# Optimization experiments

Hardware: AMD Instinct MI355X
Metric: run time of the kernel (lower is better)

## Reference

```python
import jax, jax.numpy as jnp
import numpy as np

MAX_LEVEL = 3
FULL_LEN = 2 ** MAX_LEVEL  # wavelet_full_len for db1, mode='zero'


def _make_patterns():
    # Per-feature input to the DWT is [v, 0, ..., 0] (scalar zero-padded to 2**j).
    # Haar/db1 'zero' DWT of that signal is v times a fixed sparse pattern:
    # cA (len 1) = v*2^(-j/2); cD_k first element = v*2^(-k/2), rest zeros.
    pats = []
    for j in range(1, MAX_LEVEL + 1):
        vec = [2.0 ** (-j / 2.0)]                      # cA, length 1
        for k in range(1, j + 1):                      # cD_1 .. cD_j
            seg = np.zeros(2 ** (j - k))
            seg[0] = 2.0 ** (-k / 2.0)
            vec.extend(seg.tolist())
        full = np.zeros(FULL_LEN, dtype=np.float32)
        arr = np.asarray(vec, dtype=np.float32)
        full[: arr.shape[0]] = arr                     # F.pad to wavelet_full_len
        pats.append(full)
    return jnp.asarray(np.stack(pats))                 # (MAX_LEVEL, FULL_LEN)

_P = _make_patterns()


def _gumbel_hard(logits, gumb):
    # F.gumbel_softmax(logits, tau=1.0, hard=True), one sample per feature row.
    y = jax.nn.softmax(logits[None, :] + gumb, axis=-1)          # (feat, L)
    hard = jax.nn.one_hot(jnp.argmax(y, axis=-1), y.shape[-1], dtype=y.dtype)
    return jax.lax.stop_gradient(hard - y) + y                   # straight-through


def _wavelet_layer(x, logits, gumb, Wnl, bnl, Wwo, bwo):
    # Collapses the per-feature/per-level torch double loop:
    # xi_wave(level j) = v * (Wnl[f] . P[j]) + bnl[f]
    a = Wnl @ _P.T                       # (feat, levels)
    w = _gumbel_hard(logits, gumb)       # (feat, levels), one-hot rows
    coeff = jnp.sum(w * a, axis=-1)      # (feat,)
    agg = x * coeff + bnl                # (B, N, feat)
    return agg @ Wwo + bwo               # linear_out


def _mix(h, res_proj):
    diff = jnp.mean((h - res_proj) ** 2)
    th = jax.nn.sigmoid(diff)
    return th * h + (1.0 - th) * res_proj


def reference(x, adj, Wres, bres,
              Wg0, bg0, Wrg0, brg0, logits0, gumb0, Wnl0, bnl0, Wwo0, bwo0, Wrw0, brw0,
              Wg1, bg1, Wrg1, brg1, logits1, gumb1, Wnl1, bnl1, Wwo1, bwo1, Wrw1, brw1):
    res = x @ Wres + bres                                        # (B,N,Dout)
    # ---- layer 0 ----
    xg = jnp.einsum('ij,bjf->bif', adj, x) @ Wg0 + bg0           # 64->256: no residual add
    xg = _mix(xg, res @ Wrg0 + brg0)
    xw = _wavelet_layer(xg, logits0, gumb0, Wnl0, bnl0, Wwo0, bwo0) + xg  # 256==256: add
    xw = _mix(xw, res @ Wrw0 + brw0)
    # ---- layer 1 ----
    xg1 = jnp.einsum('ij,bjf->bif', adj, xw) @ Wg1 + bg1 + xw    # 256==256: add
    xg1 = _mix(xg1, res @ Wrg1 + brg1)
    xw1 = _wavelet_layer(xg1, logits1, gumb1, Wnl1, bnl1, Wwo1, bwo1)     # 256->64: no add
    xw1 = _mix(xw1, res @ Wrw1 + brw1)
    return xw1


def setup_inputs() -> dict:
    key = jax.random.key(0)
    ks = jax.random.split(key, 32)
    B, N, D_in, H, D_out = 128, 512, 64, 256, 64
    s = 0.05
    inp = {
        'x': jax.random.normal(ks[0], (B, N, D_in), jnp.float32),
        'adj': jax.random.uniform(ks[1], (N, N), jnp.float32) / N,
        'Wres': jax.random.normal(ks[2], (D_in, D_out), jnp.float32) * s,
        'bres': jax.random.normal(ks[3], (D_out,), jnp.float32) * s,
        'Wg0': jax.random.normal(ks[4], (D_in, H), jnp.float32) * s,
        'bg0': jax.random.normal(ks[5], (H,), jnp.float32) * s,
        'Wrg0': jax.random.normal(ks[6], (D_out, H), jnp.float32) * s,
        'brg0': jax.random.normal(ks[7], (H,), jnp.float32) * s,
        'logits0': jax.random.normal(ks[8], (3,), jnp.float32),
        'gumb0': jax.random.gumbel(ks[9], (H, 3), jnp.float32),
        'Wnl0': jax.random.normal(ks[10], (H, FULL_LEN), jnp.float32) * s,
        'bnl0': jax.random.normal(ks[11], (H,), jnp.float32) * s,
        'Wwo0': jax.random.normal(ks[12], (H, H), jnp.float32) * s,
        'bwo0': jax.random.normal(ks[13], (H,), jnp.float32) * s,
        'Wrw0': jax.random.normal(ks[14], (D_out, H), jnp.float32) * s,
        'brw0': jax.random.normal(ks[15], (H,), jnp.float32) * s,
        'Wg1': jax.random.normal(ks[16], (H, H), jnp.float32) * s,
        'bg1': jax.random.normal(ks[17], (H,), jnp.float32) * s,
        'Wrg1': jax.random.normal(ks[18], (D_out, H), jnp.float32) * s,
        'brg1': jax.random.normal(ks[19], (H,), jnp.float32) * s,
        'logits1': jax.random.normal(ks[20], (3,), jnp.float32),
        'gumb1': jax.random.gumbel(ks[21], (H, 3), jnp.float32),
        'Wnl1': jax.random.normal(ks[22], (H, FULL_LEN), jnp.float32) * s,
        'bnl1': jax.random.normal(ks[23], (H,), jnp.float32) * s,
        'Wwo1': jax.random.normal(ks[24], (H, D_out), jnp.float32) * s,
        'bwo1': jax.random.normal(ks[25], (D_out,), jnp.float32) * s,
        'Wrw1': jax.random.normal(ks[26], (D_out, D_out), jnp.float32) * s,
        'brw1': jax.random.normal(ks[27], (D_out,), jnp.float32) * s,
    }
    return inp
```

## Files before the change

### kernel.cpp

```cpp
#include <hip/hip_runtime.h>
#include <hip/hip_bf16.h>
#include <math.h>

#define BB   128
#define NN   512
#define DIN  64
#define HH   256
#define DOUT 64
#define BNR  (BB * NN)

typedef float  f32x4  __attribute__((ext_vector_type(4)));
typedef __bf16 bf16x8 __attribute__((ext_vector_type(8)));

#define GLP(p)  ((const __attribute__((address_space(1))) void*)(p))
#define LDSP(p) ((__attribute__((address_space(3))) void*)(p))

__constant__ float PAT[3][8] = {
    {0.70710678f, 0.70710678f, 0.f, 0.f, 0.f, 0.f, 0.f, 0.f},
    {0.5f,        0.70710678f, 0.f, 0.5f, 0.f, 0.f, 0.f, 0.f},
    {0.35355339f, 0.70710678f, 0.f, 0.f, 0.f, 0.5f, 0.f, 0.35355339f}
};

__device__ __forceinline__ unsigned short f2bfu(float x) {
    __hip_bfloat16 b = __float2bfloat16(x);
    unsigned short u;
    __builtin_memcpy(&u, &b, 2);
    return u;
}
__device__ __forceinline__ float bf2f(unsigned short u) {
    unsigned int v = ((unsigned int)u) << 16;
    float f;
    __builtin_memcpy(&f, &v, 4);
    return f;
}

__device__ __forceinline__ float block_th(const float* __restrict__ partial, int np,
                                          float inv_n, float* red, int tid)
{
    float s = 0.f;
    for (int i = tid; i < np; i += 256) s += partial[i];
    red[tid] = s;
    __syncthreads();
    for (int o = 128; o > 0; o >>= 1) {
        if (tid < o) red[tid] += red[tid + o];
        __syncthreads();
    }
    float th = 1.f / (1.f + expf(-red[0] * inv_n));
    __syncthreads();
    return th;
}

template<int BM, int BN, int FM, int FN>
__device__ __forceinline__ void write_tile(char* lds, f32x4 (&a)[FM][FN],
                                           __hip_bfloat16* __restrict__ C,
                                           long base, int N, int tid)
{
    const int wave = tid >> 6;
    const int lane = tid & 63;
    const int wm = wave >> 1, wn = wave & 1;
    const int lc = lane & 15;
    const int lr4 = (lane >> 4) << 2;
    __syncthreads();
    #pragma unroll
    for (int j = 0; j < FN; ++j) {
        int colb = (wn * (FN * 16) + j * 16 + lc) * 2;
        #pragma unroll
        for (int i = 0; i < FM; ++i) {
            int row0 = wm * (FM * 16) + i * 16 + lr4;
            #pragma unroll
            for (int r = 0; r < 4; ++r) {
                int row = row0 + r;
                *reinterpret_cast<unsigned short*>(
                    lds + row * (BN * 2) + (colb ^ (((row >> 2) & 3) << 5))) =
                    f2bfu(a[i][j][r]);
            }
        }
    }
    __syncthreads();
    const int TPR = BN / 8;
    const int RPP = 256 / TPR;
    #pragma unroll
    for (int p = 0; p < BM / RPP; ++p) {
        int row = p * RPP + tid / TPR;
        int cb = (tid % TPR) * 16;
        int pb = cb ^ (((row >> 2) & 3) << 5);
        uint4 v = *reinterpret_cast<const uint4*>(lds + row * (BN * 2) + pb);
        *reinterpret_cast<uint4*>(reinterpret_cast<char*>(C + base + (long)row * N) + cb) = v;
    }
}

template<int BM, int BN, int FM, int FN>
__device__ __forceinline__ void write_tileT(char* lds, f32x4 (&a)[FM][FN],
                                            __hip_bfloat16* __restrict__ CT,
                                            long baseT, int ldT, int tid)
{
    const int wave = tid >> 6;
    const int lane = tid & 63;
    const int wm = wave >> 1, wn = wave & 1;
    const int lc = lane & 15;
    const int lr4 = (lane >> 4) << 2;
    __syncthreads();
    #pragma unroll
    for (int j = 0; j < FN; ++j) {
        int c = wn * (FN * 16) + j * 16 + lc;
        int cbase = c * (BM * 2);
        int swz = ((c >> 2) & 3) << 5;
        #pragma unroll
        for (int i = 0; i < FM; ++i) {
            int m0 = wm * (FM * 16) + i * 16 + lr4;
            #pragma unroll
            for (int r = 0; r < 4; ++r) {
                int m = m0 + r;
                *reinterpret_cast<unsigned short*>(lds + cbase + ((m * 2) ^ swz)) =
                    f2bfu(a[i][j][r]);
            }
        }
    }
    __syncthreads();
    const int TPR = BM / 8;
    const int RPP = 256 / TPR;
    #pragma unroll
    for (int p = 0; p < BN / RPP; ++p) {
        int c = p * RPP + tid / TPR;
        int tb = (tid % TPR) * 16;
        int pb = tb ^ (((c >> 2) & 3) << 5);
        uint4 v = *reinterpret_cast<const uint4*>(lds + c * (BM * 2) + pb);
        *reinterpret_cast<uint4*>(reinterpret_cast<char*>(CT + baseT + (long)c * ldT) + tb) = v;
    }
}

template<int BM, int BN>
__device__ __forceinline__ void stage_tiles(const __hip_bfloat16* __restrict__ Ab,
                                            const __hip_bfloat16* __restrict__ Bb,
                                            char* AsB, char* BsB,
                                            int m0, int n0, int k0, int KA, int KB,
                                            int wave, int lane)
{
    const int NCH = (BM + BN) / 32;
    const int lr = lane >> 3;
    const int ls = lane & 7;
    #pragma unroll
    for (int cc = 0; cc < NCH; ++cc) {
        int c = wave * NCH + cc;
        const __hip_bfloat16* src;
        char* ldsb;
        if (c < BM / 8) {
            int r = c * 8 + lr;
            ldsb = AsB + c * 1024;
            src = Ab + ((long)(m0 + r) * KA + k0 + ((ls ^ (r & 7)) << 3));
        } else {
            int c2 = c - BM / 8;
            int r = c2 * 8 + lr;
            ldsb = BsB + c2 * 1024;
            src = Bb + ((long)(n0 + r) * KB + k0 + ((ls ^ (r & 7)) << 3));
        }
        __builtin_amdgcn_global_load_lds(GLP(src), LDSP(ldsb), 16, 0, 0);
    }
}

template<int BM, int BN, int FM, int FN>
__device__ __forceinline__ void mfma_tiles(char* AsB, char* BsB,
                                           f32x4 (&acc)[FM][FN], int wave, int lane)
{
    const int wm = wave >> 1, wn = wave & 1;
    #pragma unroll
    for (int ksl = 0; ksl < 2; ++ksl) {
        bf16x8 af[FM], bfr[FN];
        #pragma unroll
        for (int i = 0; i < FM; ++i) {
            int row = wm * (FM * 16) + i * 16 + (lane & 15);
            int off = (ksl * 64 + ((lane >> 4) << 4)) ^ ((row & 7) << 4);
            af[i] = *reinterpret_cast<const bf16x8*>(AsB + row * 128 + off);
        }
        #pragma unroll
        for (int j = 0; j < FN; ++j) {
            int row = wn * (FN * 16) + j * 16 + (lane & 15);
            int off = (ksl * 64 + ((lane >> 4) << 4)) ^ ((row & 7) << 4);
            bfr[j] = *reinterpret_cast<const bf16x8*>(BsB + row * 128 + off);
        }
        #pragma unroll
        for (int i = 0; i < FM; ++i)
            #pragma unroll
            for (int j = 0; j < FN; ++j)
                acc[i][j] = __builtin_amdgcn_mfma_f32_16x16x32_bf16(
                    af[i], bfr[j], acc[i][j], 0, 0, 0);
    }
}

__global__ __launch_bounds__(256) void cvta_k(const float* __restrict__ adj,
                                              unsigned int* __restrict__ adjb,
                                              float* __restrict__ ars)
{
    int n = blockIdx.x;
    int t = threadIdx.x;
    float2 v = reinterpret_cast<const float2*>(adj)[n * 256 + t];
    adjb[n * 256 + t] = (unsigned int)f2bfu(v.x) | ((unsigned int)f2bfu(v.y) << 16);
    __shared__ float sm[256];
    sm[t] = v.x + v.y;
    __syncthreads();
    for (int o = 128; o > 0; o >>= 1) {
        if (t < o) sm[t] += sm[t + o];
        __syncthreads();
    }
    if (t == 0) ars[n] = sm[0];
}

__global__ __launch_bounds__(256) void cvtx_k(const float* __restrict__ in,
                                              unsigned short* __restrict__ rm,
                                              unsigned short* __restrict__ tr)
{
    __shared__ float t[64][65];
    const long base = (long)blockIdx.z * NN * DIN;
    const int r0 = blockIdx.y * 64;
    const int tr4 = threadIdx.x >> 6;
    const int tc  = threadIdx.x & 63;
    #pragma unroll
    for (int i = 0; i < 16; ++i) {
        int r = i * 4 + tr4;
        float v = in[base + (long)(r0 + r) * DIN + tc];
        t[r][tc] = v;
        rm[base + (long)(r0 + r) * DIN + tc] = f2bfu(v);
    }
    __syncthreads();
    #pragma unroll
    for (int i = 0; i < 16; ++i) {
        int d = i * 4 + tr4;
        tr[base + (long)d * NN + r0 + tc] = f2bfu(t[tc][d]);
    }
}

__device__ __forceinline__ void tcvt_body(const float* __restrict__ in,
                                          unsigned short* __restrict__ out,
                                          const float* __restrict__ cs, float us,
                                          int R, int C, int r0, int c0)
{
    __shared__ float t[64][65];
    int tr = threadIdx.x >> 6;
    int tc = threadIdx.x & 63;
    #pragma unroll
    for (int i = 0; i < 16; ++i) {
        int r = i * 4 + tr;
        t[r][tc] = in[(long)(r0 + r) * C + c0 + tc];
    }
    __syncthreads();
    float sc = (cs ? cs[r0 + tc] : 1.0f) * us;
    #pragma unroll
    for (int i = 0; i < 16; ++i) {
        int r = i * 4 + tr;
        out[(long)(c0 + r) * R + r0 + tc] = f2bfu(t[tc][r] * sc);
    }
}

struct WTArgs {
    const float* src[8];
    unsigned short* dst[8];
    const float* cs[8];
    float sgn[8];
    int R[8], C[8];
};
__global__ __launch_bounds__(256) void tcvt_w_k(WTArgs a)
{
    int wgt = blockIdx.y;
    int R = a.R[wgt], C = a.C[wgt];
    int tilesX = C >> 6;
    int tiles = (R >> 6) * tilesX;
    int t = blockIdx.x;
    if (t >= tiles) return;
    tcvt_body(a.src[wgt], a.dst[wgt], a.cs[wgt], a.sgn[wgt], R, C,
              (t / tilesX) * 64, (t % tilesX) * 64);
}

__global__ void coeff2_k(const float* __restrict__ logits0, const float* __restrict__ gumb0,
                         const float* __restrict__ Wnl0, float* __restrict__ c0,
                         const float* __restrict__ logits1, const float* __restrict__ gumb1,
                         const float* __restrict__ Wnl1, float* __restrict__ c1)
{
    const float* lg = blockIdx.x ? logits1 : logits0;
    const float* gb = blockIdx.x ? gumb1 : gumb0;
    const float* Wn = blockIdx.x ? Wnl1 : Wnl0;
    float* cc = blockIdx.x ? c1 : c0;
    int f = threadIdx.x;
    float l0 = lg[0] + gb[f * 3 + 0];
    float l1 = lg[1] + gb[f * 3 + 1];
    float l2 = lg[2] + gb[f * 3 + 2];
    int bl = 0;
    float bv = l0;
    if (l1 > bv) { bv = l1; bl = 1; }
    if (l2 > bv) { bv = l2; bl = 2; }
    float s = 0.f;
    #pragma unroll
    for (int t = 0; t < 8; ++t) s += Wn[f * 8 + t] * PAT[bl][t];
    cc[f] = s;
}

struct FVArgs {
    const float* W[6];
    const float* c[6];
    const float* v[6];
    const float* base[6];
    float* out[6];
    int K[6], N[6];
};
__global__ __launch_bounds__(256) void foldvec_k(FVArgs a)
{
    int cs = blockIdx.y;
    int n = blockIdx.x;
    if (n >= a.N[cs]) return;
    int k = threadIdx.x;
    float s = 0.f;
    if (k < a.K[cs]) {
        float cc = a.c[cs] ? a.c[cs][k] : 1.0f;
        s = a.v[cs][k] * cc * a.W[cs][(long)k * a.N[cs] + n];
    }
    __shared__ float sm[256];
    sm[threadIdx.x] = s;
    __syncthreads();
    for (int o = 128; o > 0; o >>= 1) {
        if (threadIdx.x < o) sm[threadIdx.x] += sm[threadIdx.x + o];
        __syncthreads();
    }
    if (threadIdx.x == 0)
        a.out[cs][n] = (a.base[cs] ? a.base[cs][n] : 0.f) + sm[0];
}

struct WFArgs {
    const float* Wsrc[4];
    const float* Wbig[4];
    const float* c[4];
    int incl[4], N[4];
    unsigned short* dst[4];
};
__global__ __launch_bounds__(256) void wfold_k(WFArgs a)
{
    int cs = blockIdx.y;
    int m = blockIdx.x;
    __shared__ float ws[256];
    const float* c = a.c[cs];
    ws[threadIdx.x] = a.Wsrc[cs][m * 256 + threadIdx.x] * (c ? c[threadIdx.x] : 1.0f);
    __syncthreads();
    int n = threadIdx.x;
    int N = a.N[cs];
    if (n >= N) return;
    float s = a.incl[cs] ? a.Wsrc[cs][m * 256 + n] : 0.f;
    const float* Wb = a.Wbig[cs];
    #pragma unroll 8
    for (int k = 0; k < 256; ++k)
        s += ws[k] * Wb[(long)k * N + n];
    a.dst[cs][n * 64 + m] = f2bfu(s);
}

__global__ __launch_bounds__(256) void sc0_k(
    const float* __restrict__ partial, int np, float inv_n,
    unsigned short* __restrict__ Wa,
    unsigned short* __restrict__ Wb,
    const float* __restrict__ bg0p, const float* __restrict__ brg0p,
    const float* __restrict__ crow0, float* __restrict__ cv0)
{
    __shared__ float red[256];
    float th = block_th(partial, np, inv_n, red, threadIdx.x);
    float om = 1.f - th;
    int g = blockIdx.x * 256 + threadIdx.x;
    Wa[g] = f2bfu(th * bf2f(Wa[g]));
    Wb[g] = f2bfu(om * bf2f(Wb[g]));
    if (g < 256) cv0[g] = th * bg0p[g] + om * brg0p[g] + crow0[g];
}

__global__ __launch_bounds__(256) void sc1_k(
    const float* __restrict__ partial, int np, float inv_n,
    unsigned short* __restrict__ Wg1T,
    const unsigned short* __restrict__ Wrw0T, unsigned short* __restrict__ Wrw0sT,
    unsigned short* __restrict__ Wg0pT, unsigned short* __restrict__ Wrg0pT,
    unsigned short* __restrict__ WrwWg1T,
    const float* __restrict__ bg1, const float* __restrict__ brw0,
    const float* __restrict__ cv0, const float* __restrict__ bw1v,
    float* __restrict__ bv1g, float* __restrict__ bw1s)
{
    __shared__ float red[256];
    float th = block_th(partial, np, inv_n, red, threadIdx.x);
    float om = 1.f - th;
    int g = blockIdx.x * 256 + threadIdx.x;
    Wg1T[g] = f2bfu(th * bf2f(Wg1T[g]));
    if (g < 16384) {
        Wrw0sT[g]  = f2bfu(om * bf2f(Wrw0T[g]));
        Wg0pT[g]   = f2bfu(th * bf2f(Wg0pT[g]));
        Wrg0pT[g]  = f2bfu(th * bf2f(Wrg0pT[g]));
        WrwWg1T[g] = f2bfu(om * bf2f(WrwWg1T[g]));
    }
    if (g < 256) {
        bv1g[g] = bg1[g] + om * brw0[g] + th * cv0[g];
        bw1s[g] = om * bw1v[g];
    }
}

__global__ __launch_bounds__(256) void sc2_k(
    const float* __restrict__ partial, int np, float inv_n,
    unsigned short* __restrict__ Wc1T,
    unsigned short* __restrict__ Wrgc1T,
    const float* __restrict__ brgc1, const float* __restrict__ crow1,
    float* __restrict__ cv2)
{
    __shared__ float red[256];
    float th = block_th(partial, np, inv_n, red, threadIdx.x);
    float om = 1.f - th;
    int g = blockIdx.x * 256 + threadIdx.x;
    Wc1T[g] = f2bfu(th * bf2f(Wc1T[g]));
    if (g < 4096) Wrgc1T[g] = f2bfu(om * bf2f(Wrgc1T[g]));
    if (g < 64) cv2[g] = om * brgc1[g] + crow1[g];
}

template<int BM, int BN, int FM, int FN>
__global__ __launch_bounds__(256) void gemm_res_k(
    const __hip_bfloat16* __restrict__ A, const __hip_bfloat16* __restrict__ Bt,
    const float* __restrict__ bias,
    __hip_bfloat16* __restrict__ Cb, __hip_bfloat16* __restrict__ CbT,
    int M, int N, int K)
{
    __shared__ __attribute__((aligned(128))) char lds[(BM + BN) * 128];
    char* AsB = lds;
    char* BsB = lds + BM * 128;

    const int m0 = blockIdx.y * BM;
    const int n0 = 0;
    const int tid  = threadIdx.x;
    const int wave = tid >> 6;
    const int lane = tid & 63;
    const int wn = wave & 1;

    f32x4 acc[FM][FN];
    #pragma unroll
    for (int i = 0; i < FM; ++i)
        #pragma unroll
        for (int j = 0; j < FN; ++j)
            acc[i][j] = (f32x4){0.f, 0.f, 0.f, 0.f};

    for (int k0 = 0; k0 < K; k0 += 64) {
        stage_tiles<BM, BN>(A, Bt, AsB, BsB, m0, n0, k0, K, K, wave, lane);
        __syncthreads();
        mfma_tiles<BM, BN, FM, FN>(AsB, BsB, acc, wave, lane);
        __syncthreads();
    }

    const int lc = lane & 15;
    #pragma unroll
    for (int j = 0; j < FN; ++j) {
        float bv = bias[n0 + wn * (FN * 16) + j * 16 + lc];
        #pragma unroll
        for (int i = 0; i < FM; ++i)
            #pragma unroll
            for (int r = 0; r < 4; ++r)
                acc[i][j][r] += bv;
    }
    write_tile<BM, BN, FM, FN>(lds, acc, Cb, (long)m0 * N + n0, N, tid);
    long baseT = (long)(m0 / NN) * ((long)N * NN) + (m0 % NN);
    write_tileT<BM, BN, FM, FN>(lds, acc, CbT, baseT, NN, tid);
}

template<int BM, int BN, int FM, int FN, int GX, int NB>
__global__ __launch_bounds__(256) void gemm_bt_swz_k(
    const __hip_bfloat16* __restrict__ A, const __hip_bfloat16* __restrict__ Bt,
    __hip_bfloat16* __restrict__ Cb,
    int M, int N, int K, long sA, long sB, long sC)
{
    __shared__ __attribute__((aligned(128))) char lds[(BM + BN) * 128];
    char* AsB = lds;
    char* BsB = lds + BM * 128;

    const int d   = blockIdx.x;
    const int xcd = d & 7;
    const int q   = d >> 3;
    const int t   = q % NB;
    const int bz  = xcd + ((q / NB) << 3);
    const int n0  = (t % GX) * BN;
    const int m0  = (t / GX) * BM;

    const __hip_bfloat16* Ab = A + (long)bz * sA;
    const __hip_bfloat16* Bb = Bt + (long)bz * sB;

    const int tid  = threadIdx.x;
    const int wave = tid >> 6;
    const int lane = tid & 63;

    f32x4 acc[FM][FN];
    #pragma unroll
    for (int i = 0; i < FM; ++i)
        #pragma unroll
        for (int j = 0; j < FN; ++j)
            acc[i][j] = (f32x4){0.f, 0.f, 0.f, 0.f};

    for (int k0 = 0; k0 < K; k0 += 64) {
        stage_tiles<BM, BN>(Ab, Bb, AsB, BsB, m0, n0, k0, K, K, wave, lane);
        __syncthreads();
        mfma_tiles<BM, BN, FM, FN>(AsB, BsB, acc, wave, lane);
        __syncthreads();
    }

    write_tile<BM, BN, FM, FN>(lds, acc, Cb, (long)bz * sC + (long)m0 * N + n0, N, tid);
}

template<int BM, int BN, int FM, int FN>
__global__ __launch_bounds__(256) void dual1_k(
    const __hip_bfloat16* __restrict__ A0, const __hip_bfloat16* __restrict__ B0, int K0,
    const __hip_bfloat16* __restrict__ A1, const __hip_bfloat16* __restrict__ B1, int K1,
    const float* __restrict__ b1, const float* __restrict__ b2,
    float* __restrict__ partial, int M, int N)
{
    __shared__ __attribute__((aligned(128))) char lds[(BM + BN) * 128];
    char* AsB = lds;
    char* BsB = lds + BM * 128;

    const int d   = blockIdx.x;
    const int q   = d >> 3;
    const int nx  = q & 1;
    const int my  = (d & 7) + ((q >> 1) << 3);
    const int m0  = my * BM;
    const int n0  = nx * BN;

    const int tid  = threadIdx.x;
    const int wave = tid >> 6;
    const int lane = tid & 63;
    const int wn = wave & 1;

    f32x4 acc[FM][FN];
    #pragma unroll
    for (int i = 0; i < FM; ++i)
        #pragma unroll
        for (int j = 0; j < FN; ++j)
            acc[i][j] = (f32x4){0.f, 0.f, 0.f, 0.f};

    #pragma unroll
    for (int ph = 0; ph < 2; ++ph) {
        const __hip_bfloat16* Ab = ph ? A1 : A0;
        const __hip_bfloat16* Bb = ph ? B1 : B0;
        const int K = ph ? K1 : K0;
        for (int k0 = 0; k0 < K; k0 += 64) {
            stage_tiles<BM, BN>(Ab, Bb, AsB, BsB, m0, n0, k0, K, K, wave, lane);
            __syncthreads();
            mfma_tiles<BM, BN, FM, FN>(AsB, BsB, acc, wave, lane);
            __syncthreads();
        }
    }

    const int lc = lane & 15;
    float dsum = 0.f;
    #pragma unroll
    for (int j = 0; j < FN; ++j) {
        int col = n0 + wn * (FN * 16) + j * 16 + lc;
        float bd = b1[col] - b2[col];
        #pragma unroll
        for (int i = 0; i < FM; ++i)
            #pragma unroll
            for (int r = 0; r < 4; ++r) {
                float dd = acc[i][j][r] + bd;
                dsum += dd * dd;
            }
    }

    float* red = (float*)lds;
    red[tid] = dsum;
    __syncthreads();
    for (int o = 128; o > 0; o >>= 1) {
        if (tid < o) red[tid] += red[tid + o];
        __syncthreads();
    }
    if (tid == 0) partial[my * 2 + nx] = red[0];
}

template<int BM, int BN, int FM, int FN>
__global__ __launch_bounds__(256) void wave2T_k(
    const __hip_bfloat16* __restrict__ A0, const __hip_bfloat16* __restrict__ B0, int K0,
    const __hip_bfloat16* __restrict__ A1, const __hip_bfloat16* __restrict__ B1, int K1,
    const __hip_bfloat16* __restrict__ A2, const __hip_bfloat16* __restrict__ B2, int K2,
    const float* __restrict__ cv, const float* __restrict__ b2v,
    __hip_bfloat16* __restrict__ C1T, float* __restrict__ partial_out, int M, int N)
{
    __shared__ __attribute__((aligned(128))) char lds[(BM + BN) * 128];
    char* AsB = lds;
    char* BsB = lds + BM * 128;

    const int d   = blockIdx.x;
    const int q   = d >> 3;
    const int nx  = q & 1;
    const int my  = (d & 7) + ((q >> 1) << 3);
    const int m0  = my * BM;
    const int n0  = nx * BN;

    const int tid  = threadIdx.x;
    const int wave = tid >> 6;
    const int lane = tid & 63;
    const int wn = wave & 1;

    f32x4 acc0[FM][FN], acc1[FM][FN];
    #pragma unroll
    for (int i = 0; i < FM; ++i)
        #pragma unroll
        for (int j = 0; j < FN; ++j) {
            acc0[i][j] = (f32x4){0.f, 0.f, 0.f, 0.f};
            acc1[i][j] = (f32x4){0.f, 0.f, 0.f, 0.f};
        }

    #pragma unroll
    for (int ph = 0; ph < 3; ++ph) {
        const __hip_bfloat16* Ab = (ph == 0) ? A0 : (ph == 1 ? A1 : A2);
        const __hip_bfloat16* Bb = (ph == 0) ? B0 : (ph == 1 ? B1 : B2);
        const int K = (ph == 0) ? K0 : (ph == 1 ? K1 : K2);
        for (int k0 = 0; k0 < K; k0 += 64) {
            stage_tiles<BM, BN>(Ab, Bb, AsB, BsB, m0, n0, k0, K, K, wave, lane);
            __syncthreads();
            if (ph < 2) mfma_tiles<BM, BN, FM, FN>(AsB, BsB, acc0, wave, lane);
            else        mfma_tiles<BM, BN, FM, FN>(AsB, BsB, acc1, wave, lane);
            __syncthreads();
        }
    }

    const int lc = lane & 15;
    float dsum = 0.f;
    #pragma unroll
    for (int j = 0; j < FN; ++j) {
        int col = n0 + wn * (FN * 16) + j * 16 + lc;
        float c1 = cv[col];
        float c2 = b2v[col];
        #pragma unroll
        for (int i = 0; i < FM; ++i)
            #pragma unroll
            for (int r = 0; r < 4; ++r) {
                float v1 = acc0[i][j][r] + c1;
                float v2 = acc1[i][j][r] + c2;
                acc0[i][j][r] = v1;
                float dd = v1 - v2;
                dsum += dd * dd;
            }
    }

    float* red = (float*)lds;
    red[tid] = dsum;
    __syncthreads();
    for (int o = 128; o > 0; o >>= 1) {
        if (tid < o) red[tid] += red[tid + o];
        __syncthreads();
    }
    if (tid == 0) partial_out[my * 2 + nx] = red[0];

    long baseT = (long)(m0 / NN) * ((long)N * NN) + (long)n0 * NN + (m0 % NN);
    write_tileT<BM, BN, FM, FN>(lds, acc0, C1T, baseT, NN, tid);
}

template<int BM, int BN, int FM, int FN>
__global__ __launch_bounds__(256) void gmix4_k(
    const __hip_bfloat16* __restrict__ A0, const __hip_bfloat16* __restrict__ B0, int K0,
    const __hip_bfloat16* __restrict__ A1, const __hip_bfloat16* __restrict__ B1, int K1,
    const __hip_bfloat16* __restrict__ A2, const __hip_bfloat16* __restrict__ B2, int K2,
    const __hip_bfloat16* __restrict__ A3, const __hip_bfloat16* __restrict__ B3, int K3,
    const __hip_bfloat16* __restrict__ A4, const __hip_bfloat16* __restrict__ B4, int K4,
    const __hip_bfloat16* __restrict__ A5, const __hip_bfloat16* __restrict__ B5, int K5,
    const float* __restrict__ bv1, const float* __restrict__ b2v,
    const float* __restrict__ ars, const float* __restrict__ bw1s,
    __hip_bfloat16* __restrict__ C1, float* __restrict__ partial_out, int M, int N)
{
    __shared__ __attribute__((aligned(128))) char lds[(BM + BN) * 128];
    char* AsB = lds;
    char* BsB = lds + BM * 128;

    const int d  = blockIdx.x;
    const int q  = d >> 3;
    const int nx = q & 1;
    const int my = (d & 7) + ((q >> 1) << 3);
    const int m0 = my * BM;
    const int n0 = nx * BN;

    const int tid  = threadIdx.x;
    const int wave = tid >> 6;
    const int lane = tid & 63;
    const int wm = wave >> 1, wn = wave & 1;

    f32x4 acc0[FM][FN], acc1[FM][FN];
    #pragma unroll
    for (int i = 0; i < FM; ++i)
        #pragma unroll
        for (int j = 0; j < FN; ++j) {
            acc0[i][j] = (f32x4){0.f, 0.f, 0.f, 0.f};
            acc1[i][j] = (f32x4){0.f, 0.f, 0.f, 0.f};
        }

    const __hip_bfloat16* As[6] = {A0, A1, A2, A3, A4, A5};
    const __hip_bfloat16* Bs[6] = {B0, B1, B2, B3, B4, B5};
    const int Ks[6] = {K0, K1, K2, K3, K4, K5};

    #pragma unroll
    for (int ph = 0; ph < 6; ++ph) {
        const __hip_bfloat16* Ab = As[ph];
        const __hip_bfloat16* Bb = Bs[ph];
        const int K = Ks[ph];
        for (int k0 = 0; k0 < K; k0 += 64) {
            stage_tiles<BM, BN>(Ab, Bb, AsB, BsB, m0, n0, k0, K, K, wave, lane);
            __syncthreads();
            if (ph < 5) mfma_tiles<BM, BN, FM, FN>(AsB, BsB, acc0, wave, lane);
            else        mfma_tiles<BM, BN, FM, FN>(AsB, BsB, acc1, wave, lane);
            __syncthreads();
        }
    }

    const int lc  = lane & 15;
    const int lr4 = (lane >> 4) << 2;
    const int node0 = m0 & (NN - 1);
    float dsum = 0.f;
    #pragma unroll
    for (int j = 0; j < FN; ++j) {
        int col = n0 + wn * (FN * 16) + j * 16 + lc;
        float c1 = bv1[col];
        float c2 = b2v[col];
        float bw = bw1s[col];
        #pragma unroll
        for (int i = 0; i < FM; ++i) {
            int rowl = wm * (FM * 16) + i * 16 + lr4;
            #pragma unroll
            for (int r = 0; r < 4; ++r) {
                float av = ars[node0 + rowl + r];
                float v1 = acc0[i][j][r] + c1 + av * bw;
                float v2 = acc1[i][j][r] + c2;
                acc0[i][j][r] = v1;
                float dd = v1 - v2;
                dsum += dd * dd;
            }
        }
    }

    float* red = (float*)lds;
    red[tid] = dsum;
    __syncthreads();
    for (int o = 128; o > 0; o >>= 1) {
        if (tid < o) red[tid] += red[tid + o];
        __syncthreads();
    }
    if (tid == 0) partial_out[my * 2 + nx] = red[0];

    write_tile<BM, BN, FM, FN>(lds, acc0, C1, (long)m0 * N + n0, N, tid);
}

template<int BM, int BN, int FM, int FN>
__global__ __launch_bounds__(256) void wave2_k(
    const __hip_bfloat16* __restrict__ A0, const __hip_bfloat16* __restrict__ B0, int K0,
    const __hip_bfloat16* __restrict__ A1, const __hip_bfloat16* __restrict__ B1, int K1,
    const __hip_bfloat16* __restrict__ A2, const __hip_bfloat16* __restrict__ B2, int K2,
    const float* __restrict__ cv, const float* __restrict__ b2v,
    __hip_bfloat16* __restrict__ C1, __hip_bfloat16* __restrict__ C2,
    float* __restrict__ partial_out, int M, int N)
{
    __shared__ __attribute__((aligned(128))) char lds[(BM + BN) * 128];
    char* AsB = lds;
    char* BsB = lds + BM * 128;

    const int m0 = blockIdx.y * BM;
    const int n0 = blockIdx.x * BN;
    const int pidx = blockIdx.y * gridDim.x + blockIdx.x;

    const int tid  = threadIdx.x;
    const int wave = tid >> 6;
    const int lane = tid & 63;
    const int wn = wave & 1;

    f32x4 acc0[FM][FN], acc1[FM][FN];
    #pragma unroll
    for (int i = 0; i < FM; ++i)
        #pragma unroll
        for (int j = 0; j < FN; ++j) {
            acc0[i][j] = (f32x4){0.f, 0.f, 0.f, 0.f};
            acc1[i][j] = (f32x4){0.f, 0.f, 0.f, 0.f};
        }

    #pragma unroll
    for (int ph = 0; ph < 3; ++ph) {
        const __hip_bfloat16* Ab = (ph == 0) ? A0 : (ph == 1 ? A1 : A2);
        const __hip_bfloat16* Bb = (ph == 0) ? B0 : (ph == 1 ? B1 : B2);
        const int K = (ph == 0) ? K0 : (ph == 1 ? K1 : K2);
        for (int k0 = 0; k0 < K; k0 += 64) {
            stage_tiles<BM, BN>(Ab, Bb, AsB, BsB, m0, n0, k0, K, K, wave, lane);
            __syncthreads();
            if (ph < 2) mfma_tiles<BM, BN, FM, FN>(AsB, BsB, acc0, wave, lane);
            else        mfma_tiles<BM, BN, FM, FN>(AsB, BsB, acc1, wave, lane);
            __syncthreads();
        }
    }

    const int lc = lane & 15;
    float dsum = 0.f;
    #pragma unroll
    for (int j = 0; j < FN; ++j) {
        int col = n0 + wn * (FN * 16) + j * 16 + lc;
        float c1 = cv[col];
        float c2 = b2v[col];
        #pragma unroll
        for (int i = 0; i < FM; ++i)
            #pragma unroll
            for (int r = 0; r < 4; ++r) {
                float v1 = acc0[i][j][r] + c1;
                float v2 = acc1[i][j][r] + c2;
                acc0[i][j][r] = v1;
                acc1[i][j][r] = v2;
                float dd = v1 - v2;
                dsum += dd * dd;
            }
    }

    float* red = (float*)lds;
    red[tid] = dsum;
    __syncthreads();
    for (int o = 128; o > 0; o >>= 1) {
        if (tid < o) red[tid] += red[tid + o];
        __syncthreads();
    }
    if (tid == 0) partial_out[pidx] = red[0];

    write_tile<BM, BN, FM, FN>(lds, acc0, C1, (long)m0 * N + n0, N, tid);
    write_tile<BM, BN, FM, FN>(lds, acc1, C2, (long)m0 * N + n0, N, tid);
}

__global__ __launch_bounds__(256) void mixfinal_k(
    const unsigned short* __restrict__ h, const unsigned short* __restrict__ r,
    const float* __restrict__ partial_in, int np_in, float inv_in,
    float* __restrict__ out, long n4)
{
    __shared__ float sm[256];
    const float th = block_th(partial_in, np_in, inv_in, sm, (int)threadIdx.x);
    const float om = 1.f - th;
    long gid = (long)blockIdx.x * 256 + threadIdx.x;
    long stride = (long)gridDim.x * 256;
    for (long i = gid; i < n4; i += stride) {
        ushort4 hv = reinterpret_cast<const ushort4*>(h)[i];
        ushort4 rv = reinterpret_cast<const ushort4*>(r)[i];
        float4 o;
        o.x = th * bf2f(hv.x) + om * bf2f(rv.x);
        o.y = th * bf2f(hv.y) + om * bf2f(rv.y);
        o.z = th * bf2f(hv.z) + om * bf2f(rv.z);
        o.w = th * bf2f(hv.w) + om * bf2f(rv.w);
        reinterpret_cast<float4*>(out)[i] = o;
    }
}

extern "C" void kernel_launch(void* const* d_in, const int* in_sizes, int n_in,
                              void* d_out, int out_size, void* d_ws, size_t ws_size,
                              hipStream_t stream)
{
    const float* x       = (const float*)d_in[0];
    const float* adj     = (const float*)d_in[1];
    const float* Wres    = (const float*)d_in[2];
    const float* bres    = (const float*)d_in[3];
    const float* Wg0     = (const float*)d_in[4];
    const float* bg0     = (const float*)d_in[5];
    const float* Wrg0    = (const float*)d_in[6];
    const float* brg0    = (const float*)d_in[7];
    const float* logits0 = (const float*)d_in[8];
    const float* gumb0   = (const float*)d_in[9];
    const float* Wnl0    = (const float*)d_in[10];
    const float* bnl0    = (const float*)d_in[11];
    const float* Wwo0    = (const float*)d_in[12];
    const float* bwo0    = (const float*)d_in[13];
    const float* Wrw0    = (const float*)d_in[14];
    const float* brw0    = (const float*)d_in[15];
    const float* Wg1     = (const float*)d_in[16];
    const float* bg1     = (const float*)d_in[17];
    const float* Wrg1    = (const float*)d_in[18];
    const float* brg1    = (const float*)d_in[19];
    const float* logits1 = (const float*)d_in[20];
    const float* gumb1   = (const float*)d_in[21];
    const float* Wnl1    = (const float*)d_in[22];
    const float* bnl1    = (const float*)d_in[23];
    const float* Wwo1    = (const float*)d_in[24];
    const float* bwo1    = (const float*)d_in[25];
    const float* Wrw1    = (const float*)d_in[26];
    const float* brw1    = (const float*)d_in[27];

    float* out = (float*)d_out;

    char* w = (char*)d_ws;
    auto alloc = [&](long bytes) { char* p = w; w += (bytes + 255) & ~255L; return p; };
    const long SLOT = (long)BNR * HH * 2;
    char* pool = alloc(5 * SLOT);
    __hip_bfloat16* Rbf  = (__hip_bfloat16*)alloc((long)BNR * DOUT * 2);
    __hip_bfloat16* adjb = (__hip_bfloat16*)alloc((long)NN * NN * 2);
    __hip_bfloat16* WT   = (__hip_bfloat16*)alloc(225280L * 2);
    float* partial0 = (float*)alloc(2048 * 4);
    float* partial1 = (float*)alloc(2048 * 4);
    float* partial2 = (float*)alloc(2048 * 4);
    float* partial3 = (float*)alloc(2048 * 4);
    float* c0      = (float*)alloc(256 * 4);
    float* c1      = (float*)alloc(256 * 4);
    float* bg0p    = (float*)alloc(256 * 4);
    float* brg0p   = (float*)alloc(256 * 4);
    float* crow0   = (float*)alloc(256 * 4);
    float* brgc1   = (float*)alloc(64 * 4);
    float* crow1   = (float*)alloc(64 * 4);
    float* cv0     = (float*)alloc(256 * 4);
    float* bv1g    = (float*)alloc(256 * 4);
    float* cv2     = (float*)alloc(64 * 4);
    float* ars     = (float*)alloc(512 * 4);
    float* bw1v    = (float*)alloc(256 * 4);
    float* bw1s    = (float*)alloc(256 * 4);

    auto S = [&](int i) { return pool + (long)i * SLOT; };
    __hip_bfloat16* xwrT = (__hip_bfloat16*)S(0);
    __hip_bfloat16* orw  = (__hip_bfloat16*)S(1);
    __hip_bfloat16* rw1  = (__hip_bfloat16*)(S(1) + (long)BNR * DOUT * 2);
    __hip_bfloat16* Radj = (__hip_bfloat16*)(S(1) + 2L * BNR * DOUT * 2);
    __hip_bfloat16* xg1  = (__hip_bfloat16*)S(2);
    __hip_bfloat16* T1x  = (__hip_bfloat16*)S(3);
    __hip_bfloat16* xbf  = (__hip_bfloat16*)S(4);
    __hip_bfloat16* xT   = (__hip_bfloat16*)(S(4) + (long)BNR * DIN * 2);
    __hip_bfloat16* T0   = (__hip_bfloat16*)(S(4) + 2L * BNR * DIN * 2);
    __hip_bfloat16* RbfT = (__hip_bfloat16*)(S(4) + 3L * BNR * DIN * 2);

    __hip_bfloat16* WresT   = WT;
    __hip_bfloat16* Wg0T    = WT + 4096;
    __hip_bfloat16* Wrg0T   = WT + 20480;
    __hip_bfloat16* Wrw0T   = WT + 36864;
    __hip_bfloat16* Wg1T    = WT + 53248;
    __hip_bfloat16* Wrg1T   = WT + 118784;
    __hip_bfloat16* Wc1T    = WT + 135168;
    __hip_bfloat16* Wrw1T   = WT + 151552;
    __hip_bfloat16* Wg0pT   = WT + 155648;
    __hip_bfloat16* Wrg0pT  = WT + 172032;
    __hip_bfloat16* Wrgc1T  = WT + 188416;
    __hip_bfloat16* Wrw0sT  = WT + 192512;
    __hip_bfloat16* WrwWg1T = WT + 208896;

    const dim3 blk(256);
    const float invH = 1.0f / ((float)BNR * HH);
    const float invD = 1.0f / ((float)BNR * DOUT);

    hipLaunchKernelGGL(coeff2_k, dim3(2), dim3(256), 0, stream,
                       logits0, gumb0, Wnl0, c0, logits1, gumb1, Wnl1, c1);
    hipLaunchKernelGGL(cvta_k, dim3(NN), blk, 0, stream, adj, (unsigned int*)adjb, ars);
    hipLaunchKernelGGL(cvtx_k, dim3(1, 8, BB), blk, 0, stream, x,
                       (unsigned short*)xbf, (unsigned short*)xT);

    WTArgs wa;
    wa.src[0] = Wres; wa.dst[0] = (unsigned short*)WresT; wa.cs[0] = nullptr; wa.sgn[0] = 1.f;  wa.R[0] = 64;  wa.C[0] = 64;
    wa.src[1] = Wg0;  wa.dst[1] = (unsigned short*)Wg0T;  wa.cs[1] = nullptr; wa.sgn[1] = 1.f;  wa.R[1] = 64;  wa.C[1] = 256;
    wa.src[2] = Wrg0; wa.dst[2] = (unsigned short*)Wrg0T; wa.cs[2] = nullptr; wa.sgn[2] = -1.f; wa.R[2] = 64;  wa.C[2] = 256;
    wa.src[3] = Wrw0; wa.dst[3] = (unsigned short*)Wrw0T; wa.cs[3] = nullptr; wa.sgn[3] = 1.f;  wa.R[3] = 64;  wa.C[3] = 256;
    wa.src[4] = Wg1;  wa.dst[4] = (unsigned short*)Wg1T;  wa.cs[4] = nullptr; wa.sgn[4] = 1.f;  wa.R[4] = 256; wa.C[4] = 256;
    wa.src[5] = Wrg1; wa.dst[5] = (unsigned short*)Wrg1T; wa.cs[5] = nullptr; wa.sgn[5] = 1.f;  wa.R[5] = 64;  wa.C[5] = 256;
    wa.src[6] = Wwo1; wa.dst[6] = (unsigned short*)Wc1T;  wa.cs[6] = c1;      wa.sgn[6] = 1.f;  wa.R[6] = 256; wa.C[6] = 64;
    wa.src[7] = Wrw1; wa.dst[7] = (unsigned short*)Wrw1T; wa.cs[7] = nullptr; wa.sgn[7] = 1.f;  wa.R[7] = 64;  wa.C[7] = 64;
    hipLaunchKernelGGL(tcvt_w_k, dim3(16, 8), blk, 0, stream, wa);

    WFArgs wf;
    wf.Wsrc[0] = Wg0;  wf.Wbig[0] = Wwo0; wf.c[0] = c0;      wf.incl[0] = 1; wf.N[0] = 256;
    wf.dst[0] = (unsigned short*)Wg0pT;
    wf.Wsrc[1] = Wrg0; wf.Wbig[1] = Wwo0; wf.c[1] = c0;      wf.incl[1] = 1; wf.N[1] = 256;
    wf.dst[1] = (unsigned short*)Wrg0pT;
    wf.Wsrc[2] = Wrg1; wf.Wbig[2] = Wwo1; wf.c[2] = c1;      wf.incl[2] = 0; wf.N[2] = 64;
    wf.dst[2] = (unsigned short*)Wrgc1T;
    wf.Wsrc[3] = Wrw0; wf.Wbig[3] = Wg1;  wf.c[3] = nullptr; wf.incl[3] = 0; wf.N[3] = 256;
    wf.dst[3] = (unsigned short*)WrwWg1T;
    hipLaunchKernelGGL(wfold_k, dim3(64, 4), blk, 0, stream, wf);

    FVArgs fv;
    fv.W[0] = Wwo0; fv.c[0] = c0;      fv.v[0] = bg0;  fv.base[0] = bg0;     fv.out[0] = bg0p;  fv.K[0] = 256; fv.N[0] = 256;
    fv.W[1] = Wwo0; fv.c[1] = c0;      fv.v[1] = brg0; fv.base[1] = brg0;    fv.out[1] = brg0p; fv.K[1] = 256; fv.N[1] = 256;
    fv.W[2] = Wwo0; fv.c[2] = nullptr; fv.v[2] = bnl0; fv.base[2] = bwo0;    fv.out[2] = crow0; fv.K[2] = 256; fv.N[2] = 256;
    fv.W[3] = Wwo1; fv.c[3] = c1;      fv.v[3] = brg1; fv.base[3] = nullptr; fv.out[3] = brgc1; fv.K[3] = 256; fv.N[3] = 64;
    fv.W[4] = Wwo1; fv.c[4] = nullptr; fv.v[4] = bnl1; fv.base[4] = bwo1;    fv.out[4] = crow1; fv.K[4] = 256; fv.N[4] = 64;
    fv.W[5] = Wg1;  fv.c[5] = nullptr; fv.v[5] = brw0; fv.base[5] = nullptr; fv.out[5] = bw1v;  fv.K[5] = 256; fv.N[5] = 256;
    hipLaunchKernelGGL(foldvec_k, dim3(256, 6), blk, 0, stream, fv);

    hipLaunchKernelGGL((gemm_res_k<128, 64, 4, 2>), dim3(1, BNR / 128, 1), blk, 0, stream,
                       xbf, WresT, bres, Rbf, RbfT, BNR, DOUT, DIN);

    hipLaunchKernelGGL((gemm_bt_swz_k<128, 64, 4, 2, 1, 4>), dim3(BB * 4), blk, 0, stream,
                       adjb, xT, T0, NN, DIN, NN, 0, (long)DIN * NN, (long)NN * DIN);

    hipLaunchKernelGGL((gemm_bt_swz_k<128, 64, 4, 2, 1, 4>), dim3(BB * 4), blk, 0, stream,
                       adjb, RbfT, Radj, NN, DOUT, NN, 0, (long)DOUT * NN, (long)NN * DOUT);

    hipLaunchKernelGGL((dual1_k<64, 128, 2, 4>), dim3(2 * BNR / 64), blk, 0, stream,
                       T0, Wg0T, DIN, Rbf, Wrg0T, DOUT, bg0, brg0, partial0, BNR, HH);

    hipLaunchKernelGGL(sc0_k, dim3(64), blk, 0, stream, partial0, 2048, invH,
                       (unsigned short*)Wg0pT, (unsigned short*)Wrg0pT,
                       bg0p, brg0p, crow0, cv0);

    hipLaunchKernelGGL((wave2T_k<64, 128, 2, 4>), dim3(2 * BNR / 64), blk, 0, stream,
                       T0, Wg0pT, DIN, Rbf, Wrg0pT, DOUT, Rbf, Wrw0T, DOUT,
                       cv0, brw0, xwrT, partial1, BNR, HH);

    hipLaunchKernelGGL(sc1_k, dim3(256), blk, 0, stream, partial1, 2048, invH,
                       (unsigned short*)Wg1T,
                       (const unsigned short*)Wrw0T, (unsigned short*)Wrw0sT,
                       (unsigned short*)Wg0pT, (unsigned short*)Wrg0pT,
                       (unsigned short*)WrwWg1T,
                       bg1, brw0, cv0, bw1v, bv1g, bw1s);

    hipLaunchKernelGGL((gemm_bt_swz_k<128, 128, 4, 4, 2, 8>), dim3(BB * 8), blk, 0, stream,
                       adjb, xwrT, T1x, NN, HH, NN, 0, (long)HH * NN, (long)NN * HH);

    hipLaunchKernelGGL((gmix4_k<64, 128, 2, 4>), dim3(2 * BNR / 64), blk, 0, stream,
                       T1x, Wg1T, HH,
                       Radj, WrwWg1T, DOUT,
                       T0, Wg0pT, DIN,
                       Rbf, Wrg0pT, DOUT,
                       Rbf, Wrw0sT, DOUT,
                       Rbf, Wrg1T, DOUT,
                       bv1g, brg1, ars, bw1s, xg1, partial2, BNR, HH);

    hipLaunchKernelGGL(sc2_k, dim3(64), blk, 0, stream, partial2, 2048, invH,
                       (unsigned short*)Wc1T, (unsigned short*)Wrgc1T,
                       brgc1, crow1, cv2);

    hipLaunchKernelGGL((wave2_k<64, 64, 2, 2>), dim3(1, BNR / 64), blk, 0, stream,
                       xg1, Wc1T, HH, Rbf, Wrgc1T, DOUT, Rbf, Wrw1T, DIN,
                       cv2, brw1, orw, rw1, partial3, BNR, DOUT);

    hipLaunchKernelGGL(mixfinal_k, dim3(2048), blk, 0, stream,
                       (const unsigned short*)orw, (const unsigned short*)rw1,
                       partial3, 1024, invD, out, (long)BNR * DOUT / 4);
}
```

Measured before the change: 194.2 us.

## Double-buffer LDS staging across GEMM phases and merge two residual weight products

Adds a shared pipe_run helper that double-buffers LDS tiles. The next K-slice, or the next phase's operands, is staged while MFMAs run on the current buffer, so each step needs one barrier instead of two. All fused GEMM kernels now use it, which doubles their LDS footprint. sc1_k folds the scaled Wrg0p and Wrw0 weights into one combined matrix, so gmix drops from six operand phases to five. The adj×xwr GEMM also moves to 128x64 tiles on a larger grid.

```diff
diff --git a/kernel.cpp b/kernel.cpp
--- a/kernel.cpp
+++ b/kernel.cpp
@@ -187,6 +187,32 @@
     }
 }
 
+template<int BM, int BN, int FM, int FN, int NS, int NA>
+__device__ __forceinline__ void pipe_run(
+    const __hip_bfloat16* const (&sA)[NS], const __hip_bfloat16* const (&sB)[NS],
+    const int (&sK)[NS], const int (&sk0)[NS],
+    char* buf0, char* buf1,
+    f32x4 (&acc0)[FM][FN], f32x4 (&acc1)[FM][FN],
+    int m0, int n0, int wave, int lane)
+{
+    constexpr int BOFF = BM * 128;
+    stage_tiles<BM, BN>(sA[0], sB[0], buf0, buf0 + BOFF, m0, n0, sk0[0],
+                        sK[0], sK[0], wave, lane);
+    __syncthreads();
+    #pragma unroll
+    for (int t = 0; t < NS; ++t) {
+        char* bc = (t & 1) ? buf1 : buf0;
+        if (t + 1 < NS) {
+            char* bn = (t & 1) ? buf0 : buf1;
+            stage_tiles<BM, BN>(sA[t + 1], sB[t + 1], bn, bn + BOFF, m0, n0,
+                                sk0[t + 1], sK[t + 1], sK[t + 1], wave, lane);
+        }
+        if (t < NA) mfma_tiles<BM, BN, FM, FN>(bc, bc + BOFF, acc0, wave, lane);
+        else        mfma_tiles<BM, BN, FM, FN>(bc, bc + BOFF, acc1, wave, lane);
+        __syncthreads();
+    }
+}
+
 __global__ __launch_bounds__(256) void cvta_k(const float* __restrict__ adj,
                                               unsigned int* __restrict__ adjb,
                                               float* __restrict__ ars)
@@ -368,8 +394,9 @@
 __global__ __launch_bounds__(256) void sc1_k(
     const float* __restrict__ partial, int np, float inv_n,
     unsigned short* __restrict__ Wg1T,
-    const unsigned short* __restrict__ Wrw0T, unsigned short* __restrict__ Wrw0sT,
-    unsigned short* __restrict__ Wg0pT, unsigned short* __restrict__ Wrg0pT,
+    const unsigned short* __restrict__ Wrw0T, const unsigned short* __restrict__ Wrg0pT,
+    unsigned short* __restrict__ WcombT,
+    unsigned short* __restrict__ Wg0pT,
     unsigned short* __restrict__ WrwWg1T,
     const float* __restrict__ bg1, const float* __restrict__ brw0,
     const float* __restrict__ cv0, const float* __restrict__ bw1v,
@@ -381,9 +408,8 @@
     int g = blockIdx.x * 256 + threadIdx.x;
     Wg1T[g] = f2bfu(th * bf2f(Wg1T[g]));
     if (g < 16384) {
-        Wrw0sT[g]  = f2bfu(om * bf2f(Wrw0T[g]));
+        WcombT[g]  = f2bfu(th * bf2f(Wrg0pT[g]) + om * bf2f(Wrw0T[g]));
         Wg0pT[g]   = f2bfu(th * bf2f(Wg0pT[g]));
-        Wrg0pT[g]  = f2bfu(th * bf2f(Wrg0pT[g]));
         WrwWg1T[g] = f2bfu(om * bf2f(WrwWg1T[g]));
     }
     if (g < 256) {
@@ -420,7 +446,6 @@
     char* BsB = lds + BM * 128;
 
     const int m0 = blockIdx.y * BM;
-    const int n0 = 0;
     const int tid  = threadIdx.x;
     const int wave = tid >> 6;
     const int lane = tid & 63;
@@ -434,7 +459,7 @@
             acc[i][j] = (f32x4){0.f, 0.f, 0.f, 0.f};
 
     for (int k0 = 0; k0 < K; k0 += 64) {
-        stage_tiles<BM, BN>(A, Bt, AsB, BsB, m0, n0, k0, K, K, wave, lane);
+        stage_tiles<BM, BN>(A, Bt, AsB, BsB, m0, 0, k0, K, K, wave, lane);
         __syncthreads();
         mfma_tiles<BM, BN, FM, FN>(AsB, BsB, acc, wave, lane);
         __syncthreads();
@@ -443,27 +468,25 @@
     const int lc = lane & 15;
     #pragma unroll
     for (int j = 0; j < FN; ++j) {
-        float bv = bias[n0 + wn * (FN * 16) + j * 16 + lc];
+        float bv = bias[wn * (FN * 16) + j * 16 + lc];
         #pragma unroll
         for (int i = 0; i < FM; ++i)
             #pragma unroll
             for (int r = 0; r < 4; ++r)
                 acc[i][j][r] += bv;
     }
-    write_tile<BM, BN, FM, FN>(lds, acc, Cb, (long)m0 * N + n0, N, tid);
+    write_tile<BM, BN, FM, FN>(lds, acc, Cb, (long)m0 * N, N, tid);
     long baseT = (long)(m0 / NN) * ((long)N * NN) + (m0 % NN);
     write_tileT<BM, BN, FM, FN>(lds, acc, CbT, baseT, NN, tid);
 }
 
-template<int BM, int BN, int FM, int FN, int GX, int NB>
+template<int BM, int BN, int FM, int FN, int GX, int NB, int NS>
 __global__ __launch_bounds__(256) void gemm_bt_swz_k(
     const __hip_bfloat16* __restrict__ A, const __hip_bfloat16* __restrict__ Bt,
     __hip_bfloat16* __restrict__ Cb,
     int M, int N, int K, long sA, long sB, long sC)
 {
-    __shared__ __attribute__((aligned(128))) char lds[(BM + BN) * 128];
-    char* AsB = lds;
-    char* BsB = lds + BM * 128;
+    __shared__ __attribute__((aligned(128))) char lds[2 * (BM + BN) * 128];
 
     const int d   = blockIdx.x;
     const int xcd = d & 7;
@@ -487,12 +510,15 @@
         for (int j = 0; j < FN; ++j)
             acc[i][j] = (f32x4){0.f, 0.f, 0.f, 0.f};
 
-    for (int k0 = 0; k0 < K; k0 += 64) {
-        stage_tiles<BM, BN>(Ab, Bb, AsB, BsB, m0, n0, k0, K, K, wave, lane);
-        __syncthreads();
-        mfma_tiles<BM, BN, FM, FN>(AsB, BsB, acc, wave, lane);
-        __syncthreads();
-    }
+    const __hip_bfloat16* pA[NS];
+    const __hip_bfloat16* pB[NS];
+    int pK[NS], pk0[NS];
+    #pragma unroll
+    for (int s = 0; s < NS; ++s) { pA[s] = Ab; pB[s] = Bb; pK[s] = K; pk0[s] = s * 64; }
+
+    pipe_run<BM, BN, FM, FN, NS, NS>(pA, pB, pK, pk0,
+                                     lds, lds + (BM + BN) * 128,
+                                     acc, acc, m0, n0, wave, lane);
 
     write_tile<BM, BN, FM, FN>(lds, acc, Cb, (long)bz * sC + (long)m0 * N + n0, N, tid);
 }
@@ -504,9 +530,7 @@
     const float* __restrict__ b1, const float* __restrict__ b2,
     float* __restrict__ partial, int M, int N)
 {
-    __shared__ __attribute__((aligned(128))) char lds[(BM + BN) * 128];
-    char* AsB = lds;
-    char* BsB = lds + BM * 128;
+    __shared__ __attribute__((aligned(128))) char lds[2 * (BM + BN) * 128];
 
     const int d   = blockIdx.x;
     const int q   = d >> 3;
@@ -527,18 +551,13 @@
         for (int j = 0; j < FN; ++j)
             acc[i][j] = (f32x4){0.f, 0.f, 0.f, 0.f};
 
-    #pragma unroll
-    for (int ph = 0; ph < 2; ++ph) {
-        const __hip_bfloat16* Ab = ph ? A1 : A0;
-        const __hip_bfloat16* Bb = ph ? B1 : B0;
-        const int K = ph ? K1 : K0;
-        for (int k0 = 0; k0 < K; k0 += 64) {
-            stage_tiles<BM, BN>(Ab, Bb, AsB, BsB, m0, n0, k0, K, K, wave, lane);
-            __syncthreads();
-            mfma_tiles<BM, BN, FM, FN>(AsB, BsB, acc, wave, lane);
-            __syncthreads();
-        }
-    }
+    const __hip_bfloat16* pA[2] = {A0, A1};
+    const __hip_bfloat16* pB[2] = {B0, B1};
+    int pK[2] = {K0, K1};
+    int pk0[2] = {0, 0};
+    pipe_run<BM, BN, FM, FN, 2, 2>(pA, pB, pK, pk0,
+                                   lds, lds + (BM + BN) * 128,
+                                   acc, acc, m0, n0, wave, lane);
 
     const int lc = lane & 15;
     float dsum = 0.f;
@@ -573,9 +592,7 @@
     const float* __restrict__ cv, const float* __restrict__ b2v,
     __hip_bfloat16* __restrict__ C1T, float* __restrict__ partial_out, int M, int N)
 {
-    __shared__ __attribute__((aligned(128))) char lds[(BM + BN) * 128];
-    char* AsB = lds;
-    char* BsB = lds + BM * 128;
+    __shared__ __attribute__((aligned(128))) char lds[2 * (BM + BN) * 128];
 
     const int d   = blockIdx.x;
     const int q   = d >> 3;
@@ -598,19 +615,13 @@
             acc1[i][j] = (f32x4){0.f, 0.f, 0.f, 0.f};
         }
 
-    #pragma unroll
-    for (int ph = 0; ph < 3; ++ph) {
-        const __hip_bfloat16* Ab = (ph == 0) ? A0 : (ph == 1 ? A1 : A2);
-        const __hip_bfloat16* Bb = (ph == 0) ? B0 : (ph == 1 ? B1 : B2);
-        const int K = (ph == 0) ? K0 : (ph == 1 ? K1 : K2);
-        for (int k0 = 0; k0 < K; k0 += 64) {
-            stage_tiles<BM, BN>(Ab, Bb, AsB, BsB, m0, n0, k0, K, K, wave, lane);
-            __syncthreads();
-            if (ph < 2) mfma_tiles<BM, BN, FM, FN>(AsB, BsB, acc0, wave, lane);
-            else        mfma_tiles<BM, BN, FM, FN>(AsB, BsB, acc1, wave, lane);
-            __syncthreads();
-        }
-    }
+    const __hip_bfloat16* pA[3] = {A0, A1, A2};
+    const __hip_bfloat16* pB[3] = {B0, B1, B2};
+    int pK[3] = {K0, K1, K2};
+    int pk0[3] = {0, 0, 0};
+    pipe_run<BM, BN, FM, FN, 3, 2>(pA, pB, pK, pk0,
+                                   lds, lds + (BM + BN) * 128,
+                                   acc0, acc1, m0, n0, wave, lane);
 
     const int lc = lane & 15;
     float dsum = 0.f;
@@ -645,20 +656,17 @@
 }
 
 template<int BM, int BN, int FM, int FN>
-__global__ __launch_bounds__(256) void gmix4_k(
+__global__ __launch_bounds__(256) void gmix5_k(
     const __hip_bfloat16* __restrict__ A0, const __hip_bfloat16* __restrict__ B0, int K0,
     const __hip_bfloat16* __restrict__ A1, const __hip_bfloat16* __restrict__ B1, int K1,
     const __hip_bfloat16* __restrict__ A2, const __hip_bfloat16* __restrict__ B2, int K2,
     const __hip_bfloat16* __restrict__ A3, const __hip_bfloat16* __restrict__ B3, int K3,
     const __hip_bfloat16* __restrict__ A4, const __hip_bfloat16* __restrict__ B4, int K4,
-    const __hip_bfloat16* __restrict__ A5, const __hip_bfloat16* __restrict__ B5, int K5,
     const float* __restrict__ bv1, const float* __restrict__ b2v,
     const float* __restrict__ ars, const float* __restrict__ bw1s,
     __hip_bfloat16* __restrict__ C1, float* __restrict__ partial_out, int M, int N)
 {
-    __shared__ __attribute__((aligned(128))) char lds[(BM + BN) * 128];
-    char* AsB = lds;
-    char* BsB = lds + BM * 128;
+    __shared__ __attribute__((aligned(128))) char lds[2 * (BM + BN) * 128];
 
     const int d  = blockIdx.x;
     const int q  = d >> 3;
@@ -681,23 +689,13 @@
             acc1[i][j] = (f32x4){0.f, 0.f, 0.f, 0.f};
         }
 
-    const __hip_bfloat16* As[6] = {A0, A1, A2, A3, A4, A5};
-    const __hip_bfloat16* Bs[6] = {B0, B1, B2, B3, B4, B5};
-    const int Ks[6] = {K0, K1, K2, K3, K4, K5};
-
-    #pragma unroll
-    for (int ph = 0; ph < 6; ++ph) {
-        const __hip_bfloat16* Ab = As[ph];
-        const __hip_bfloat16* Bb = Bs[ph];
-        const int K = Ks[ph];
-        for (int k0 = 0; k0 < K; k0 += 64) {
-            stage_tiles<BM, BN>(Ab, Bb, AsB, BsB, m0, n0, k0, K, K, wave, lane);
-            __syncthreads();
-            if (ph < 5) mfma_tiles<BM, BN, FM, FN>(AsB, BsB, acc0, wave, lane);
-            else        mfma_tiles<BM, BN, FM, FN>(AsB, BsB, acc1, wave, lane);
-            __syncthreads();
-        }
-    }
+    const __hip_bfloat16* pA[8] = {A0, A0, A0, A0, A1, A2, A3, A4};
+    const __hip_bfloat16* pB[8] = {B0, B0, B0, B0, B1, B2, B3, B4};
+    int pK[8]  = {K0, K0, K0, K0, K1, K2, K3, K4};
+    int pk0[8] = {0, 64, 128, 192, 0, 0, 0, 0};
+    pipe_run<BM, BN, FM, FN, 8, 7>(pA, pB, pK, pk0,
+                                   lds, lds + (BM + BN) * 128,
+                                   acc0, acc1, m0, n0, wave, lane);
 
     const int lc  = lane & 15;
     const int lr4 = (lane >> 4) << 2;
@@ -745,9 +743,7 @@
     __hip_bfloat16* __restrict__ C1, __hip_bfloat16* __restrict__ C2,
     float* __restrict__ partial_out, int M, int N)
 {
-    __shared__ __attribute__((aligned(128))) char lds[(BM + BN) * 128];
-    char* AsB = lds;
-    char* BsB = lds + BM * 128;
+    __shared__ __attribute__((aligned(128))) char lds[2 * (BM + BN) * 128];
 
     const int m0 = blockIdx.y * BM;
     const int n0 = blockIdx.x * BN;
@@ -767,19 +763,13 @@
             acc1[i][j] = (f32x4){0.f, 0.f, 0.f, 0.f};
         }
 
-    #pragma unroll
-    for (int ph = 0; ph < 3; ++ph) {
-        const __hip_bfloat16* Ab = (ph == 0) ? A0 : (ph == 1 ? A1 : A2);
-        const __hip_bfloat16* Bb = (ph == 0) ? B0 : (ph == 1 ? B1 : B2);
-        const int K = (ph == 0) ? K0 : (ph == 1 ? K1 : K2);
-        for (int k0 = 0; k0 < K; k0 += 64) {
-            stage_tiles<BM, BN>(Ab, Bb, AsB, BsB, m0, n0, k0, K, K, wave, lane);
-            __syncthreads();
-            if (ph < 2) mfma_tiles<BM, BN, FM, FN>(AsB, BsB, acc0, wave, lane);
-            else        mfma_tiles<BM, BN, FM, FN>(AsB, BsB, acc1, wave, lane);
-            __syncthreads();
-        }
-    }
+    const __hip_bfloat16* pA[6] = {A0, A0, A0, A0, A1, A2};
+    const __hip_bfloat16* pB[6] = {B0, B0, B0, B0, B1, B2};
+    int pK[6]  = {K0, K0, K0, K0, K1, K2};
+    int pk0[6] = {0, 64, 128, 192, 0, 0};
+    pipe_run<BM, BN, FM, FN, 6, 5>(pA, pB, pK, pk0,
+                                   lds, lds + (BM + BN) * 128,
+                                   acc0, acc1, m0, n0, wave, lane);
 
     const int lc = lane & 15;
     float dsum = 0.f;
@@ -919,7 +909,7 @@
     __hip_bfloat16* Wg0pT   = WT + 155648;
     __hip_bfloat16* Wrg0pT  = WT + 172032;
     __hip_bfloat16* Wrgc1T  = WT + 188416;
-    __hip_bfloat16* Wrw0sT  = WT + 192512;
+    __hip_bfloat16* WcombT  = WT + 192512;
     __hip_bfloat16* WrwWg1T = WT + 208896;
 
     const dim3 blk(256);
@@ -966,10 +956,10 @@
     hipLaunchKernelGGL((gemm_res_k<128, 64, 4, 2>), dim3(1, BNR / 128, 1), blk, 0, stream,
                        xbf, WresT, bres, Rbf, RbfT, BNR, DOUT, DIN);
 
-    hipLaunchKernelGGL((gemm_bt_swz_k<128, 64, 4, 2, 1, 4>), dim3(BB * 4), blk, 0, stream,
+    hipLaunchKernelGGL((gemm_bt_swz_k<128, 64, 4, 2, 1, 4, 8>), dim3(BB * 4), blk, 0, stream,
                        adjb, xT, T0, NN, DIN, NN, 0, (long)DIN * NN, (long)NN * DIN);
 
-    hipLaunchKernelGGL((gemm_bt_swz_k<128, 64, 4, 2, 1, 4>), dim3(BB * 4), blk, 0, stream,
+    hipLaunchKernelGGL((gemm_bt_swz_k<128, 64, 4, 2, 1, 4, 8>), dim3(BB * 4), blk, 0, stream,
                        adjb, RbfT, Radj, NN, DOUT, NN, 0, (long)DOUT * NN, (long)NN * DOUT);
 
     hipLaunchKernelGGL((dual1_k<64, 128, 2, 4>), dim3(2 * BNR / 64), blk, 0, stream,
@@ -985,20 +975,20 @@
 
     hipLaunchKernelGGL(sc1_k, dim3(256), blk, 0, stream, partial1, 2048, invH,
                        (unsigned short*)Wg1T,
-                       (const unsigned short*)Wrw0T, (unsigned short*)Wrw0sT,
-                       (unsigned short*)Wg0pT, (unsigned short*)Wrg0pT,
+                       (const unsigned short*)Wrw0T, (const unsigned short*)Wrg0pT,
+                       (unsigned short*)WcombT,
+                       (unsigned short*)Wg0pT,
                        (unsigned short*)WrwWg1T,
                        bg1, brw0, cv0, bw1v, bv1g, bw1s);
 
-    hipLaunchKernelGGL((gemm_bt_swz_k<128, 128, 4, 4, 2, 8>), dim3(BB * 8), blk, 0, stream,
+    hipLaunchKernelGGL((gemm_bt_swz_k<128, 64, 4, 2, 4, 16, 8>), dim3(BB * 16), blk, 0, stream,
                        adjb, xwrT, T1x, NN, HH, NN, 0, (long)HH * NN, (long)NN * HH);
 
-    hipLaunchKernelGGL((gmix4_k<64, 128, 2, 4>), dim3(2 * BNR / 64), blk, 0, stream,
+    hipLaunchKernelGGL((gmix5_k<64, 128, 2, 4>), dim3(2 * BNR / 64), blk, 0, stream,
                        T1x, Wg1T, HH,
                        Radj, WrwWg1T, DOUT,
                        T0, Wg0pT, DIN,
-                       Rbf, Wrg0pT, DOUT,
-                       Rbf, Wrw0sT, DOUT,
+                       Rbf, WcombT, DOUT,
                        Rbf, Wrg1T, DOUT,
                        bv1g, brg1, ars, bw1s, xg1, partial2, BNR, HH);
 
```

Result: faster. 178.2 us (-8.2%).
